# Kernel tuning notes

Measured on AMD Instinct MI355X. Metric: run time of the kernel, lower is better.

## Reference

```python
import jax, jax.numpy as jnp
import numpy as np

# Static sizes (RED-GNN on ICEWS14-like graph)
B = 32          # batch (queries)
N = 100000      # active nodes per layer (fixed frontier size)
E = 1000000     # edges per layer
H = 64          # hidden_dim
A = 5           # attn_dim
L = 3           # n_layer
N_REL = 230
N_ENT = 7128
N_TIME = 365


def setup_inputs() -> dict:
    key = jax.random.key(0)
    ks = jax.random.split(key, 16)
    inp = {}
    # edge structure (constant w.r.t. differentiation)
    inp['batch_idx'] = jax.random.randint(ks[0], (E,), 0, B)
    inp['src_idx'] = jax.random.randint(ks[1], (E,), 0, N)
    inp['dst_idx'] = jax.random.randint(ks[2], (E,), 0, N)
    inp['rel_idx'] = jax.random.randint(ks[3], (E,), 0, N_REL + 1)
    # signed relative time in [-(N_TIME-1), N_TIME-1]
    inp['rel_time'] = jax.random.randint(ks[4], (E,), -(N_TIME - 1), N_TIME)
    inp['query_rel'] = jax.random.randint(ks[5], (B,), 0, N_REL + 1)
    # unique (batch, entity) slot per final node
    n = jnp.arange(N)
    inp['out_batch'] = n // N_ENT
    inp['out_ent'] = n % N_ENT
    # learned parameters
    s = 1.0 / np.sqrt(H)
    inp['rela_embed'] = jax.random.normal(ks[6], (L, N_REL + 1, H), jnp.float32) * s
    inp['time_embed'] = jax.random.normal(ks[7], (N_TIME, H), jnp.float32) * s
    inp['Wp'] = jax.random.normal(ks[8], (H, H), jnp.float32) * s
    inp['Wn'] = jax.random.normal(ks[9], (H, H), jnp.float32) * s
    inp['Wf'] = jax.random.normal(ks[10], (H, H), jnp.float32) * s
    inp['W1'] = jax.random.normal(ks[11], (L, A, 3 * H), jnp.float32) * s
    inp['W2'] = jax.random.normal(ks[12], (L, 1, A), jnp.float32) / np.sqrt(A)
    inp['Wc'] = jax.random.normal(ks[13], (1, H), jnp.float32) * s
    inp['bc'] = jnp.zeros((1,), jnp.float32)
    return inp


def reference(rela_embed, time_embed, Wp, Wn, Wf, W1, W2, Wc, bc,
              batch_idx, src_idx, dst_idx, rel_idx, rel_time,
              query_rel, out_batch, out_ent):
    hidden = jnp.zeros((N, H), dtype=rela_embed.dtype)
    q_rel_e = query_rel[batch_idx]                 # [E]
    t_emb = time_embed[jnp.abs(rel_time)]          # [E,H]
    pos = (rel_time > 0)[:, None]
    zer = (rel_time == 0)[:, None]
    for i in range(L):
        rel_e = rela_embed[i][rel_idx]             # [E,H]
        embed = hidden[src_idx] + rel_e + t_emb    # [E,H]
        # branch by sign of relative time: future / now / past linear
        transformed = jnp.where(pos, embed @ Wf.T,
                      jnp.where(zer, embed @ Wn.T, embed @ Wp.T))
        attn_in = jnp.concatenate(
            [hidden[src_idx], rel_e, rela_embed[i][q_rel_e]], axis=1)  # [E,3H]
        score = jax.nn.sigmoid(
            jax.nn.relu(attn_in @ W1[i].T) @ W2[i].T)  # [E,1]
        msg = score * transformed                      # [E,H]
        hidden = jax.nn.relu(
            jax.ops.segment_sum(msg, dst_idx, num_segments=N))
    result = (hidden @ Wc.T + bc).reshape(-1)          # [N]
    score_all = jnp.zeros((B, N_ENT), result.dtype)
    score_all = score_all.at[out_batch, out_ent].set(result)
    return score_all
```

## Files before the change

### kernel.cpp

```cpp
#include <hip/hip_runtime.h>

#define NB   32
#define NN   100000
#define NE   1000000
#define HD   64
#define AD   5
#define NL   3
#define NRL  231
#define NTM  365
#define NOUT 228096
#define NBLK1 391
#define BLKN 32
#define NBLK2 3125


__device__ __forceinline__ float bflo(unsigned u) { return __uint_as_float(u << 16); }
__device__ __forceinline__ float bfhi(unsigned u) { return __uint_as_float(u & 0xffff0000u); }
__device__ __forceinline__ unsigned packbf2(float x, float y) {
    unsigned ux = __float_as_uint(x), uy = __float_as_uint(y);
    ux = (ux + 0x7fffu + ((ux >> 16) & 1u)) >> 16;
    uy = (uy + 0x7fffu + ((uy >> 16) & 1u)) >> 16;
    return ux | (uy << 16);
}

using vbf8  = __attribute__((ext_vector_type(8))) short;
using f32x4 = __attribute__((ext_vector_type(4))) float;

__global__ __launch_bounds__(256) void prep_wtb_kernel(
    const float* __restrict__ Wp, const float* __restrict__ Wn,
    const float* __restrict__ Wf, ushort* __restrict__ WTB)
{
    int i = blockIdx.x * 256 + threadIdx.x;
    if (i >= 3072) return;
    int lane = i & 63;
    int nt = (i >> 6) & 3;
    int ks = (i >> 8) & 1;
    int hl = (i >> 9) & 1;
    int c  = i >> 10;
    const float* W = (c == 0) ? Wf : (c == 1 ? Wn : Wp);
    int h  = nt * 16 + (lane & 15);
    int k0 = ks * 32 + (lane >> 4) * 8;
    unsigned up[4];
    #pragma unroll
    for (int j = 0; j < 4; ++j) {
        float x = W[h * 64 + k0 + 2 * j];
        float y = W[h * 64 + k0 + 2 * j + 1];
        unsigned pb = packbf2(x, y);
        if (hl) {
            float rx = x - bflo(pb);
            float ry = y - bfhi(pb);
            pb = packbf2(rx, ry);
        }
        up[j] = pb;
    }
    *(uint4*)(WTB + (size_t)i * 8) = make_uint4(up[0], up[1], up[2], up[3]);
}

__global__ __launch_bounds__(256) void prep_tb_kernel(
    const float* __restrict__ rela_embed,
    const float* __restrict__ time_embed,
    ushort* __restrict__ relb,
    ushort* __restrict__ tembb)
{
    const int nrel_w = 3 * NRL * HD / 2;
    const int ntmb_w = NTM * HD / 2;
    int i = blockIdx.x * 256 + threadIdx.x;
    if (i < nrel_w) {
        ((unsigned*)relb)[i] = packbf2(rela_embed[2 * i], rela_embed[2 * i + 1]);
    } else if (i < nrel_w + ntmb_w) {
        int k = i - nrel_w;
        ((unsigned*)tembb)[k] = packbf2(time_embed[2 * k], time_embed[2 * k + 1]);
    }
}

__global__ __launch_bounds__(256) void prep_tables_kernel(
    const float* __restrict__ rela_embed,
    const float* __restrict__ W1,
    float* __restrict__ Trel,
    float* __restrict__ Tq)
{
    int l = blockIdx.x;
    int r = threadIdx.x;
    if (r >= NRL) return;
    const float4* rrow = (const float4*)(rela_embed + ((size_t)l * NRL + r) * HD);
    const float* W1l = W1 + (size_t)l * AD * 192;
    float tr[AD] = {0,0,0,0,0}, tq[AD] = {0,0,0,0,0};
    #pragma unroll
    for (int k4 = 0; k4 < 16; ++k4) {
        float4 x = rrow[k4];
        #pragma unroll
        for (int a = 0; a < AD; ++a) {
            const float* wr = W1l + a * 192 + 64 + k4 * 4;
            const float* wq = W1l + a * 192 + 128 + k4 * 4;
            tr[a] = fmaf(x.x, wr[0], tr[a]); tr[a] = fmaf(x.y, wr[1], tr[a]);
            tr[a] = fmaf(x.z, wr[2], tr[a]); tr[a] = fmaf(x.w, wr[3], tr[a]);
            tq[a] = fmaf(x.x, wq[0], tq[a]); tq[a] = fmaf(x.y, wq[1], tq[a]);
            tq[a] = fmaf(x.z, wq[2], tq[a]); tq[a] = fmaf(x.w, wq[3], tq[a]);
        }
    }
    float* tro = Trel + ((size_t)l * NRL + r) * 8;
    float* tqo = Tq   + ((size_t)l * NRL + r) * 8;
    #pragma unroll
    for (int a = 0; a < AD; ++a) { tro[a] = tr[a]; tqo[a] = tq[a]; }
    tro[5] = tro[6] = tro[7] = 0.f;
    tqo[5] = tqo[6] = tqo[7] = 0.f;
}

__global__ __launch_bounds__(256) void hist_kernel(
    const int* __restrict__ dst_idx, int* __restrict__ deg,
    ushort* __restrict__ rank)
{
    int e = blockIdx.x * 256 + threadIdx.x;
    if (e < NE) rank[e] = (ushort)atomicAdd(&deg[dst_idx[e]], 1);
}

__global__ __launch_bounds__(256) void scan1_kernel(
    const int* __restrict__ deg, int* __restrict__ tmp, int* __restrict__ bsum)
{
    __shared__ int s[256];
    int tid = threadIdx.x;
    int i = blockIdx.x * 256 + tid;
    int v = (i < NN) ? deg[i] : 0;
    s[tid] = v;
    __syncthreads();
    #pragma unroll
    for (int st = 1; st < 256; st <<= 1) {
        int t = (tid >= st) ? s[tid - st] : 0;
        __syncthreads();
        s[tid] += t;
        __syncthreads();
    }
    if (i < NN) tmp[i] = s[tid];
    if (tid == 255) bsum[blockIdx.x] = s[255];
}

__global__ __launch_bounds__(512) void scan2_kernel(
    const int* __restrict__ bsum, int* __restrict__ bpref)
{
    __shared__ int s[512];
    int tid = threadIdx.x;
    int v = (tid < NBLK1) ? bsum[tid] : 0;
    s[tid] = v;
    __syncthreads();
    #pragma unroll
    for (int st = 1; st < 512; st <<= 1) {
        int t = (tid >= st) ? s[tid - st] : 0;
        __syncthreads();
        s[tid] += t;
        __syncthreads();
    }
    if (tid < NBLK1) bpref[tid] = s[tid] - v;
}

__global__ __launch_bounds__(256) void scan3_kernel(
    const int* __restrict__ deg, const int* __restrict__ tmp,
    const int* __restrict__ bpref, int* __restrict__ off)
{
    int i = blockIdx.x * 256 + threadIdx.x;
    if (i >= NN) return;
    int incl = tmp[i] + bpref[i >> 8];
    off[i + 1] = incl;
    if (i == 0) off[0] = 0;
}

__global__ __launch_bounds__(256) void sort_scatter_kernel(
    const int* __restrict__ dst_idx, const int* __restrict__ src_idx,
    const int* __restrict__ rel_idx, const int* __restrict__ rel_time,
    const int* __restrict__ batch_idx, const int* __restrict__ query_rel,
    const int* __restrict__ off, const ushort* __restrict__ rank,
    const float* __restrict__ Trel0, const float* __restrict__ Tq0,
    const float* __restrict__ W2,
    int2* __restrict__ meta, float* __restrict__ score0)
{
    int e = blockIdx.x * 256 + threadIdx.x;
    if (e >= NE) return;
    int d = dst_idx[e];
    int rt = rel_time[e];
    int cls = (rt > 0) ? 0 : ((rt == 0) ? 1 : 2);
    int ta = (rt < 0) ? -rt : rt;
    int rel = rel_idx[e];
    int q = query_rel[batch_idx[e]];
    int pos = off[d] + (int)rank[e];
    int2 m;
    m.x = src_idx[e] | (rel << 17) | (cls << 25);
    m.y = ta | (q << 9);
    meta[pos] = m;

    float4 t0 = *(const float4*)(Trel0 + rel * 8);
    float  t4 = Trel0[rel * 8 + 4];
    float4 u0 = *(const float4*)(Tq0 + q * 8);
    float  u4 = Tq0[q * 8 + 4];
    float z = 0.f;
    z = fmaf(fmaxf(t0.x + u0.x, 0.f), W2[0], z);
    z = fmaf(fmaxf(t0.y + u0.y, 0.f), W2[1], z);
    z = fmaf(fmaxf(t0.z + u0.z, 0.f), W2[2], z);
    z = fmaf(fmaxf(t0.w + u0.w, 0.f), W2[3], z);
    z = fmaf(fmaxf(t4   + u4,   0.f), W2[4], z);
    score0[pos] = 1.f / (1.f + __expf(-z));
}

__global__ __launch_bounds__(256) void score_kernel(
    const float* __restrict__ proj,
    const float* __restrict__ Trel,
    const float* __restrict__ Tq,
    const float* __restrict__ W2,
    const int2* __restrict__ meta,
    float* __restrict__ score)
{
    int j = blockIdx.x * 256 + threadIdx.x;
    if (j >= NE) return;
    int2 mt = meta[j];
    int rel = (mt.x >> 17) & 0xFF;
    int q   = (mt.y >> 9) & 0xFF;
    int src = mt.x & 0x1FFFF;

    float4 t0 = *(const float4*)(Trel + rel * 8);
    float  t4 = Trel[rel * 8 + 4];
    float4 u0 = *(const float4*)(Tq + q * 8);
    float  u4 = Tq[q * 8 + 4];
    float4 p0 = *(const float4*)(proj + (size_t)src * 8);
    float  p4 = proj[(size_t)src * 8 + 4];
    float z = 0.f;
    z = fmaf(fmaxf(p0.x + t0.x + u0.x, 0.f), W2[0], z);
    z = fmaf(fmaxf(p0.y + t0.y + u0.y, 0.f), W2[1], z);
    z = fmaf(fmaxf(p0.z + t0.z + u0.z, 0.f), W2[2], z);
    z = fmaf(fmaxf(p0.w + t0.w + u0.w, 0.f), W2[3], z);
    z = fmaf(fmaxf(p4   + t4   + u4,   0.f), W2[4], z);
    score[j] = 1.f / (1.f + __expf(-z));
}

template <bool HZ>
__device__ __forceinline__ void edge_acc(
    int mx, float sc, uint4 rv, uint4 tv, uint4 hv, float4* __restrict__ A)
{
    int cl = (mx >> 25) & 3;
    float4 v0, v1;
    v0.x = bflo(rv.x) + bflo(tv.x); v0.y = bfhi(rv.x) + bfhi(tv.x);
    v0.z = bflo(rv.y) + bflo(tv.y); v0.w = bfhi(rv.y) + bfhi(tv.y);
    v1.x = bflo(rv.z) + bflo(tv.z); v1.y = bfhi(rv.z) + bfhi(tv.z);
    v1.z = bflo(rv.w) + bflo(tv.w); v1.w = bfhi(rv.w) + bfhi(tv.w);
    if (!HZ) {
        v0.x += bflo(hv.x); v0.y += bfhi(hv.x);
        v0.z += bflo(hv.y); v0.w += bfhi(hv.y);
        v1.x += bflo(hv.z); v1.y += bfhi(hv.z);
        v1.z += bflo(hv.w); v1.w += bfhi(hv.w);
    }
    float sA = (cl == 0) ? sc : 0.f;
    float sB = (cl == 1) ? sc : 0.f;
    float sC = (cl == 2) ? sc : 0.f;
    A[0].x = fmaf(sA, v0.x, A[0].x); A[0].y = fmaf(sA, v0.y, A[0].y);
    A[0].z = fmaf(sA, v0.z, A[0].z); A[0].w = fmaf(sA, v0.w, A[0].w);
    A[1].x = fmaf(sA, v1.x, A[1].x); A[1].y = fmaf(sA, v1.y, A[1].y);
    A[1].z = fmaf(sA, v1.z, A[1].z); A[1].w = fmaf(sA, v1.w, A[1].w);
    A[2].x = fmaf(sB, v0.x, A[2].x); A[2].y = fmaf(sB, v0.y, A[2].y);
    A[2].z = fmaf(sB, v0.z, A[2].z); A[2].w = fmaf(sB, v0.w, A[2].w);
    A[3].x = fmaf(sB, v1.x, A[3].x); A[3].y = fmaf(sB, v1.y, A[3].y);
    A[3].z = fmaf(sB, v1.z, A[3].z); A[3].w = fmaf(sB, v1.w, A[3].w);
    A[4].x = fmaf(sC, v0.x, A[4].x); A[4].y = fmaf(sC, v0.y, A[4].y);
    A[4].z = fmaf(sC, v0.z, A[4].z); A[4].w = fmaf(sC, v0.w, A[4].w);
    A[5].x = fmaf(sC, v1.x, A[5].x); A[5].y = fmaf(sC, v1.y, A[5].y);
    A[5].z = fmaf(sC, v1.z, A[5].z); A[5].w = fmaf(sC, v1.w, A[5].w);
}

__device__ __forceinline__ uint4 ldrow(const ushort* __restrict__ base, int row, int hc8)
{
    return *(const uint4*)(base + (size_t)row * HD + hc8);
}

#define SPITCH 68
template <bool HZ, bool PROJ>
__global__ __launch_bounds__(256, 4) void reduce_transform_kernel(
    const ushort* __restrict__ hidden_in,
    const ushort* __restrict__ relb,
    const ushort* __restrict__ tembb,
    const float* __restrict__ score,
    const int2* __restrict__ meta,
    const int*  __restrict__ off,
    const ushort* __restrict__ WTB,
    const float* __restrict__ W1next,
    ushort* __restrict__ hidden_out,
    float* __restrict__ proj_out)
{
    __shared__ float lds_t[BLKN * SPITCH];
    int tid  = threadIdx.x;
    int lane = tid & 63;
    int w    = __builtin_amdgcn_readfirstlane(tid >> 6);
    int gid  = tid >> 3;
    int hc   = tid & 7;
    int hc8  = hc * 8;
    int node0 = blockIdx.x * BLKN;
    int node  = node0 + gid;

    float4 a[6];
    #pragma unroll
    for (int c = 0; c < 6; ++c)
        a[c] = make_float4(0.f, 0.f, 0.f, 0.f);

    {
        int o0 = off[node];
        int o1 = off[node + 1];
        int j = o0;
        const uint4 zz = make_uint4(0, 0, 0, 0);
        for (; j + 4 <= o1; j += 4) {
            int2 m0 = meta[j],     m1 = meta[j + 1];
            int2 m2 = meta[j + 2], m3 = meta[j + 3];
            float s0 = score[j],     s1 = score[j + 1];
            float s2 = score[j + 2], s3 = score[j + 3];
            uint4 r0 = ldrow(relb, (m0.x >> 17) & 0xFF, hc8);
            uint4 r1 = ldrow(relb, (m1.x >> 17) & 0xFF, hc8);
            uint4 r2 = ldrow(relb, (m2.x >> 17) & 0xFF, hc8);
            uint4 r3 = ldrow(relb, (m3.x >> 17) & 0xFF, hc8);
            uint4 t0 = ldrow(tembb, m0.y & 511, hc8);
            uint4 t1 = ldrow(tembb, m1.y & 511, hc8);
            uint4 t2 = ldrow(tembb, m2.y & 511, hc8);
            uint4 t3 = ldrow(tembb, m3.y & 511, hc8);
            uint4 h0 = zz, h1 = zz, h2 = zz, h3 = zz;
            if (!HZ) {
                h0 = ldrow(hidden_in, m0.x & 0x1FFFF, hc8);
                h1 = ldrow(hidden_in, m1.x & 0x1FFFF, hc8);
                h2 = ldrow(hidden_in, m2.x & 0x1FFFF, hc8);
                h3 = ldrow(hidden_in, m3.x & 0x1FFFF, hc8);
            }
            edge_acc<HZ>(m0.x, s0, r0, t0, h0, a);
            edge_acc<HZ>(m1.x, s1, r1, t1, h1, a);
            edge_acc<HZ>(m2.x, s2, r2, t2, h2, a);
            edge_acc<HZ>(m3.x, s3, r3, t3, h3, a);
        }
        for (; j < o1; ++j) {
            int2 m0 = meta[j];
            float s0 = score[j];
            uint4 r0 = ldrow(relb, (m0.x >> 17) & 0xFF, hc8);
            uint4 t0 = ldrow(tembb, m0.y & 511, hc8);
            uint4 h0 = zz;
            if (!HZ) h0 = ldrow(hidden_in, m0.x & 0x1FFFF, hc8);
            edge_acc<HZ>(m0.x, s0, r0, t0, h0, a);
        }
    }

    unsigned* lds_u = (unsigned*)lds_t;
    int rl = lane & 15;
    int t  = lane >> 4;
    int rt = w & 1;
    int ct = w >> 1;
    f32x4 accd[2];
    accd[0] = (f32x4){0.f, 0.f, 0.f, 0.f};
    accd[1] = (f32x4){0.f, 0.f, 0.f, 0.f};

    #pragma unroll
    for (int c = 0; c < 3; ++c) {
        __syncthreads();
        {
            float4 v0 = a[2 * c];
            float4 v1 = a[2 * c + 1];
            unsigned p0 = packbf2(v0.x, v0.y);
            unsigned p1 = packbf2(v0.z, v0.w);
            unsigned p2 = packbf2(v1.x, v1.y);
            unsigned p3 = packbf2(v1.z, v1.w);
            unsigned q0 = packbf2(v0.x - bflo(p0), v0.y - bfhi(p0));
            unsigned q1 = packbf2(v0.z - bflo(p1), v0.w - bfhi(p1));
            unsigned q2 = packbf2(v1.x - bflo(p2), v1.y - bfhi(p2));
            unsigned q3 = packbf2(v1.z - bflo(p3), v1.w - bfhi(p3));
            *(uint4*)(lds_u + gid * SPITCH + hc * 4)      = make_uint4(p0, p1, p2, p3);
            *(uint4*)(lds_u + gid * SPITCH + 32 + hc * 4) = make_uint4(q0, q1, q2, q3);
        }
        __syncthreads();
        #pragma unroll
        for (int ks = 0; ks < 2; ++ks) {
            const unsigned* rowp = lds_u + (rt * 16 + rl) * SPITCH + ks * 16 + t * 4;
            vbf8 ah = *(const vbf8*)rowp;
            vbf8 al = *(const vbf8*)(rowp + 32);
            #pragma unroll
            for (int b = 0; b < 2; ++b) {
                int nt = ct * 2 + b;
                const ushort* bp = WTB +
                    (size_t)((((c * 2) * 2 + ks) * 4 + nt) * 64 + lane) * 8;
                vbf8 bh = *(const vbf8*)bp;
                vbf8 bl = *(const vbf8*)(bp + 4096);
                accd[b] = __builtin_amdgcn_mfma_f32_16x16x32_bf16(ah, bh, accd[b], 0, 0, 0);
                accd[b] = __builtin_amdgcn_mfma_f32_16x16x32_bf16(al, bh, accd[b], 0, 0, 0);
                accd[b] = __builtin_amdgcn_mfma_f32_16x16x32_bf16(ah, bl, accd[b], 0, 0, 0);
            }
        }
    }

    __syncthreads();
    #pragma unroll
    for (int b = 0; b < 2; ++b)
        #pragma unroll
        for (int i = 0; i < 4; ++i)
            lds_t[(rt * 16 + t * 4 + i) * SPITCH + (ct * 2 + b) * 16 + rl] = accd[b][i];
    __syncthreads();

    float acc8[8];
    {
        const float4* rp = (const float4*)(lds_t + gid * SPITCH + hc8);
        float4 x = rp[0], y = rp[1];
        acc8[0] = x.x; acc8[1] = x.y; acc8[2] = x.z; acc8[3] = x.w;
        acc8[4] = y.x; acc8[5] = y.y; acc8[6] = y.z; acc8[7] = y.w;
    }

    {
        ushort* outp = hidden_out + (size_t)node * 64 + hc8;
        unsigned u0 = packbf2(fmaxf(acc8[0], 0.f), fmaxf(acc8[1], 0.f));
        unsigned u1 = packbf2(fmaxf(acc8[2], 0.f), fmaxf(acc8[3], 0.f));
        unsigned u2 = packbf2(fmaxf(acc8[4], 0.f), fmaxf(acc8[5], 0.f));
        unsigned u3 = packbf2(fmaxf(acc8[6], 0.f), fmaxf(acc8[7], 0.f));
        *(uint4*)outp = make_uint4(u0, u1, u2, u3);
    }

    if (PROJ) {
        float pa[AD];
        #pragma unroll
        for (int aa = 0; aa < AD; ++aa) pa[aa] = 0.f;
        #pragma unroll
        for (int i = 0; i < 8; ++i) {
            float hv = fmaxf(acc8[i], 0.f);
            #pragma unroll
            for (int aa = 0; aa < AD; ++aa)
                pa[aa] = fmaf(hv, W1next[aa * 192 + hc8 + i], pa[aa]);
        }
        __syncthreads();
        float* lds2 = lds_t;
        #pragma unroll
        for (int aa = 0; aa < AD; ++aa)
            lds2[tid * AD + aa] = pa[aa];
        __syncthreads();
        int nd = tid >> 3, aa = tid & 7;
        float v = 0.f;
        if (aa < AD) {
            #pragma unroll
            for (int ho = 0; ho < 8; ++ho)
                v += lds2[(nd * 8 + ho) * AD + aa];
        }
        proj_out[(size_t)(node0 + nd) * 8 + aa] = v;
    }
}

__global__ __launch_bounds__(256) void out_kernel(
    const ushort* __restrict__ hidden,
    const float* __restrict__ Wc,
    const float* __restrict__ bc,
    float* __restrict__ out)
{
    int i = blockIdx.x * 256 + threadIdx.x;
    if (i >= NOUT) return;
    float r = 0.f;
    if (i < NN) {
        const uint4* h4 = (const uint4*)(hidden + (size_t)i * 64);
        float acc = 0.f;
        #pragma unroll
        for (int q = 0; q < 8; ++q) {
            uint4 hv = h4[q];
            const float* wq = Wc + q * 8;
            acc = fmaf(bflo(hv.x), wq[0], acc);
            acc = fmaf(bfhi(hv.x), wq[1], acc);
            acc = fmaf(bflo(hv.y), wq[2], acc);
            acc = fmaf(bfhi(hv.y), wq[3], acc);
            acc = fmaf(bflo(hv.z), wq[4], acc);
            acc = fmaf(bfhi(hv.z), wq[5], acc);
            acc = fmaf(bflo(hv.w), wq[6], acc);
            acc = fmaf(bfhi(hv.w), wq[7], acc);
        }
        r = acc + bc[0];
    }
    out[i] = r;
}

extern "C" void kernel_launch(void* const* d_in, const int* in_sizes, int n_in,
                              void* d_out, int out_size, void* d_ws, size_t ws_size,
                              hipStream_t stream)
{
    const int*   batch_idx  = (const int*)d_in[0];
    const int*   src_idx    = (const int*)d_in[1];
    const int*   dst_idx    = (const int*)d_in[2];
    const int*   rel_idx    = (const int*)d_in[3];
    const int*   rel_time   = (const int*)d_in[4];
    const int*   query_rel  = (const int*)d_in[5];
    const float* rela_embed = (const float*)d_in[8];
    const float* time_embed = (const float*)d_in[9];
    const float* Wp         = (const float*)d_in[10];
    const float* Wn         = (const float*)d_in[11];
    const float* Wf         = (const float*)d_in[12];
    const float* W1         = (const float*)d_in[13];
    const float* W2         = (const float*)d_in[14];
    const float* Wc         = (const float*)d_in[15];
    const float* bc         = (const float*)d_in[16];
    float* out = (float*)d_out;

    char* ws = (char*)d_ws;
    ushort* hid0  = (ushort*)(ws + 0);
    ushort* hid1  = (ushort*)(ws + 12800000);
    float* projA  = (float*)(ws + 25600000);
    float* projB  = (float*)(ws + 28800000);
    float* score  = (float*)(ws + 32000000);
    ushort* WTB   = (ushort*)(ws + 36000000);
    float* Trel   = (float*)(ws + 36100000);
    float* Tq     = (float*)(ws + 36130000);
    int*   off    = (int*)  (ws + 36160000);
    int2*  meta   = (int2*) (ws + 37400000);
    int*   deg    = (int*)  (ws + 45400000);
    ushort* relb  = (ushort*)(ws + 45800000);
    ushort* tembb = (ushort*)(ws + 45950000);
    int*   tmp    = (int*)  (ws + 46600000);
    ushort* rank  = (ushort*)(ws + 47000000);
    int*   bsum   = (int*)  (ws + 49000000);
    int*   bpref  = (int*)  (ws + 49010000);

    prep_wtb_kernel<<<12, 256, 0, stream>>>(Wp, Wn, Wf, WTB);
    prep_tb_kernel<<<133, 256, 0, stream>>>(rela_embed, time_embed, relb, tembb);
    prep_tables_kernel<<<NL, 256, 0, stream>>>(rela_embed, W1, Trel, Tq);

    hipMemsetAsync(deg, 0, NN * sizeof(int), stream);
    hist_kernel<<<(NE + 255) / 256, 256, 0, stream>>>(dst_idx, deg, rank);
    scan1_kernel<<<NBLK1, 256, 0, stream>>>(deg, tmp, bsum);
    scan2_kernel<<<1, 512, 0, stream>>>(bsum, bpref);
    scan3_kernel<<<NBLK1, 256, 0, stream>>>(deg, tmp, bpref, off);
    sort_scatter_kernel<<<(NE + 255) / 256, 256, 0, stream>>>(
        dst_idx, src_idx, rel_idx, rel_time, batch_idx, query_rel,
        off, rank, Trel, Tq, W2, meta, score);

    int grid = NBLK2;
    int sgrid = (NE + 255) / 256;
    {
        reduce_transform_kernel<true, true><<<grid, 256, 0, stream>>>(
            hid1, relb, tembb, score, meta, off,
            WTB, W1 + (size_t)1 * AD * 192, hid0, projA);
    }
    {
        score_kernel<<<sgrid, 256, 0, stream>>>(
            projA, Trel + (size_t)1 * NRL * 8, Tq + (size_t)1 * NRL * 8,
            W2 + 1 * AD, meta, score);
        reduce_transform_kernel<false, true><<<grid, 256, 0, stream>>>(
            hid0, relb + (size_t)1 * NRL * HD, tembb, score, meta, off,
            WTB, W1 + (size_t)2 * AD * 192, hid1, projB);
    }
    {
        score_kernel<<<sgrid, 256, 0, stream>>>(
            projB, Trel + (size_t)2 * NRL * 8, Tq + (size_t)2 * NRL * 8,
            W2 + 2 * AD, meta, score);
        reduce_transform_kernel<false, false><<<grid, 256, 0, stream>>>(
            hid1, relb + (size_t)2 * NRL * HD, tembb, score, meta, off,
            WTB, nullptr, hid0, nullptr);
    }

    out_kernel<<<(NOUT + 255) / 256, 256, 0, stream>>>(hid0, Wc, bc, out);
}
```

Before: 380.0 us.

## Reorder nodes by in-degree to balance per-wavefront work in reduce kernel

Adds a counting sort of destination nodes by in-degree (capped at 63) producing a permutation, and makes the reduce/transform kernel process nodes in that order. Nodes sharing a wavefront then have similar edge counts, reducing divergence where lanes wait on the longest node. Costs three small extra kernels and makes hidden/proj writes scattered by row rather than contiguous per block.

```diff
diff --git a/kernel.cpp b/kernel.cpp
--- a/kernel.cpp
+++ b/kernel.cpp
@@ -161,6 +161,41 @@
     int incl = tmp[i] + bpref[i >> 8];
     off[i + 1] = incl;
     if (i == 0) off[0] = 0;
+}
+
+__global__ __launch_bounds__(256) void drank_kernel(
+    const int* __restrict__ deg, int* __restrict__ dcnt, int* __restrict__ rank_d)
+{
+    int n = blockIdx.x * 256 + threadIdx.x;
+    if (n < NN) {
+        int d = min(deg[n], 63);
+        rank_d[n] = atomicAdd(&dcnt[d], 1);
+    }
+}
+
+__global__ __launch_bounds__(64) void dscan_kernel(
+    const int* __restrict__ dcnt, int* __restrict__ dbase)
+{
+    int tid = threadIdx.x;
+    int c = dcnt[tid];
+    int v = c;
+    #pragma unroll
+    for (int st = 1; st < 64; st <<= 1) {
+        int t = __shfl_up(v, st, 64);
+        if (tid >= st) v += t;
+    }
+    dbase[tid] = v - c;
+}
+
+__global__ __launch_bounds__(256) void dscatter_kernel(
+    const int* __restrict__ deg, const int* __restrict__ rank_d,
+    const int* __restrict__ dbase, int* __restrict__ perm)
+{
+    int n = blockIdx.x * 256 + threadIdx.x;
+    if (n < NN) {
+        int d = min(deg[n], 63);
+        perm[dbase[d] + rank_d[n]] = n;
+    }
 }
 
 __global__ __launch_bounds__(256) void sort_scatter_kernel(
@@ -276,6 +311,7 @@
     const float* __restrict__ score,
     const int2* __restrict__ meta,
     const int*  __restrict__ off,
+    const int*  __restrict__ perm,
     const ushort* __restrict__ WTB,
     const float* __restrict__ W1next,
     ushort* __restrict__ hidden_out,
@@ -289,7 +325,7 @@
     int hc   = tid & 7;
     int hc8  = hc * 8;
     int node0 = blockIdx.x * BLKN;
-    int node  = node0 + gid;
+    int node  = perm[node0 + gid];
 
     float4 a[6];
     #pragma unroll
@@ -425,14 +461,13 @@
         for (int aa = 0; aa < AD; ++aa)
             lds2[tid * AD + aa] = pa[aa];
         __syncthreads();
-        int nd = tid >> 3, aa = tid & 7;
         float v = 0.f;
-        if (aa < AD) {
+        if (hc < AD) {
             #pragma unroll
             for (int ho = 0; ho < 8; ++ho)
-                v += lds2[(nd * 8 + ho) * AD + aa];
-        }
-        proj_out[(size_t)(node0 + nd) * 8 + aa] = v;
+                v += lds2[(gid * 8 + ho) * AD + hc];
+        }
+        proj_out[(size_t)node * 8 + hc] = v;
     }
 }
 
@@ -501,20 +536,27 @@
     int*   deg    = (int*)  (ws + 45400000);
     ushort* relb  = (ushort*)(ws + 45800000);
     ushort* tembb = (ushort*)(ws + 45950000);
+    int*   perm   = (int*)  (ws + 46000000);
     int*   tmp    = (int*)  (ws + 46600000);
     ushort* rank  = (ushort*)(ws + 47000000);
     int*   bsum   = (int*)  (ws + 49000000);
     int*   bpref  = (int*)  (ws + 49010000);
+    int*   dcnt   = (int*)  (ws + 49020000);
+    int*   dbase  = (int*)  (ws + 49021000);
 
     prep_wtb_kernel<<<12, 256, 0, stream>>>(Wp, Wn, Wf, WTB);
     prep_tb_kernel<<<133, 256, 0, stream>>>(rela_embed, time_embed, relb, tembb);
     prep_tables_kernel<<<NL, 256, 0, stream>>>(rela_embed, W1, Trel, Tq);
 
     hipMemsetAsync(deg, 0, NN * sizeof(int), stream);
+    hipMemsetAsync(dcnt, 0, 64 * sizeof(int), stream);
     hist_kernel<<<(NE + 255) / 256, 256, 0, stream>>>(dst_idx, deg, rank);
     scan1_kernel<<<NBLK1, 256, 0, stream>>>(deg, tmp, bsum);
     scan2_kernel<<<1, 512, 0, stream>>>(bsum, bpref);
     scan3_kernel<<<NBLK1, 256, 0, stream>>>(deg, tmp, bpref, off);
+    drank_kernel<<<NBLK1, 256, 0, stream>>>(deg, dcnt, tmp);
+    dscan_kernel<<<1, 64, 0, stream>>>(dcnt, dbase);
+    dscatter_kernel<<<NBLK1, 256, 0, stream>>>(deg, tmp, dbase, perm);
     sort_scatter_kernel<<<(NE + 255) / 256, 256, 0, stream>>>(
         dst_idx, src_idx, rel_idx, rel_time, batch_idx, query_rel,
         off, rank, Trel, Tq, W2, meta, score);
@@ -523,7 +565,7 @@
     int sgrid = (NE + 255) / 256;
     {
         reduce_transform_kernel<true, true><<<grid, 256, 0, stream>>>(
-            hid1, relb, tembb, score, meta, off,
+            hid1, relb, tembb, score, meta, off, perm,
             WTB, W1 + (size_t)1 * AD * 192, hid0, projA);
     }
     {
@@ -531,7 +573,7 @@
             projA, Trel + (size_t)1 * NRL * 8, Tq + (size_t)1 * NRL * 8,
             W2 + 1 * AD, meta, score);
         reduce_transform_kernel<false, true><<<grid, 256, 0, stream>>>(
-            hid0, relb + (size_t)1 * NRL * HD, tembb, score, meta, off,
+            hid0, relb + (size_t)1 * NRL * HD, tembb, score, meta, off, perm,
             WTB, W1 + (size_t)2 * AD * 192, hid1, projB);
     }
     {
@@ -539,7 +581,7 @@
             projB, Trel + (size_t)2 * NRL * 8, Tq + (size_t)2 * NRL * 8,
             W2 + 2 * AD, meta, score);
         reduce_transform_kernel<false, false><<<grid, 256, 0, stream>>>(
-            hid1, relb + (size_t)2 * NRL * HD, tembb, score, meta, off,
+            hid1, relb + (size_t)2 * NRL * HD, tembb, score, meta, off, perm,
             WTB, nullptr, hid0, nullptr);
     }
 
```

New measurement: 678.0 us. 1.78x slower.

## Fuse attention score computation into edge reduce kernel via lane shuffles

Applied to the files above, without the earlier changes.

Removes the separate per-edge score kernels and the score buffer; each 8-lane node group now computes the 5-dim attention pre-activation per edge (one dim per lane) from the relation, query and projected-source tables, reduces it with xor shuffles and applies the sigmoid inline. This eliminates two kernel launches and the write/read of a 1M-entry score array per layer. In exchange it adds shuffles, scattered scalar gathers of proj per edge and longer dependency chains inside the memory-bound reduce loop, and lanes 5-7 read padded table entries.

```diff
diff --git a/kernel.cpp b/kernel.cpp
--- a/kernel.cpp
+++ b/kernel.cpp
@@ -168,9 +168,7 @@
     const int* __restrict__ rel_idx, const int* __restrict__ rel_time,
     const int* __restrict__ batch_idx, const int* __restrict__ query_rel,
     const int* __restrict__ off, const ushort* __restrict__ rank,
-    const float* __restrict__ Trel0, const float* __restrict__ Tq0,
-    const float* __restrict__ W2,
-    int2* __restrict__ meta, float* __restrict__ score0)
+    int2* __restrict__ meta)
 {
     int e = blockIdx.x * 256 + threadIdx.x;
     if (e >= NE) return;
@@ -185,48 +183,6 @@
     m.x = src_idx[e] | (rel << 17) | (cls << 25);
     m.y = ta | (q << 9);
     meta[pos] = m;
-
-    float4 t0 = *(const float4*)(Trel0 + rel * 8);
-    float  t4 = Trel0[rel * 8 + 4];
-    float4 u0 = *(const float4*)(Tq0 + q * 8);
-    float  u4 = Tq0[q * 8 + 4];
-    float z = 0.f;
-    z = fmaf(fmaxf(t0.x + u0.x, 0.f), W2[0], z);
-    z = fmaf(fmaxf(t0.y + u0.y, 0.f), W2[1], z);
-    z = fmaf(fmaxf(t0.z + u0.z, 0.f), W2[2], z);
-    z = fmaf(fmaxf(t0.w + u0.w, 0.f), W2[3], z);
-    z = fmaf(fmaxf(t4   + u4,   0.f), W2[4], z);
-    score0[pos] = 1.f / (1.f + __expf(-z));
-}
-
-__global__ __launch_bounds__(256) void score_kernel(
-    const float* __restrict__ proj,
-    const float* __restrict__ Trel,
-    const float* __restrict__ Tq,
-    const float* __restrict__ W2,
-    const int2* __restrict__ meta,
-    float* __restrict__ score)
-{
-    int j = blockIdx.x * 256 + threadIdx.x;
-    if (j >= NE) return;
-    int2 mt = meta[j];
-    int rel = (mt.x >> 17) & 0xFF;
-    int q   = (mt.y >> 9) & 0xFF;
-    int src = mt.x & 0x1FFFF;
-
-    float4 t0 = *(const float4*)(Trel + rel * 8);
-    float  t4 = Trel[rel * 8 + 4];
-    float4 u0 = *(const float4*)(Tq + q * 8);
-    float  u4 = Tq[q * 8 + 4];
-    float4 p0 = *(const float4*)(proj + (size_t)src * 8);
-    float  p4 = proj[(size_t)src * 8 + 4];
-    float z = 0.f;
-    z = fmaf(fmaxf(p0.x + t0.x + u0.x, 0.f), W2[0], z);
-    z = fmaf(fmaxf(p0.y + t0.y + u0.y, 0.f), W2[1], z);
-    z = fmaf(fmaxf(p0.z + t0.z + u0.z, 0.f), W2[2], z);
-    z = fmaf(fmaxf(p0.w + t0.w + u0.w, 0.f), W2[3], z);
-    z = fmaf(fmaxf(p4   + t4   + u4,   0.f), W2[4], z);
-    score[j] = 1.f / (1.f + __expf(-z));
 }
 
 template <bool HZ>
@@ -267,13 +223,24 @@
     return *(const uint4*)(base + (size_t)row * HD + hc8);
 }
 
+__device__ __forceinline__ float grp_sigmoid(float z)
+{
+    z += __shfl_xor(z, 1);
+    z += __shfl_xor(z, 2);
+    z += __shfl_xor(z, 4);
+    return 1.f / (1.f + __expf(-z));
+}
+
 #define SPITCH 68
 template <bool HZ, bool PROJ>
 __global__ __launch_bounds__(256, 4) void reduce_transform_kernel(
     const ushort* __restrict__ hidden_in,
     const ushort* __restrict__ relb,
     const ushort* __restrict__ tembb,
-    const float* __restrict__ score,
+    const float* __restrict__ proj_in,
+    const float* __restrict__ TrelS,
+    const float* __restrict__ TqS,
+    const float* __restrict__ W2S,
     const int2* __restrict__ meta,
     const int*  __restrict__ off,
     const ushort* __restrict__ WTB,
@@ -290,6 +257,7 @@
     int hc8  = hc * 8;
     int node0 = blockIdx.x * BLKN;
     int node  = node0 + gid;
+    float w2l = (hc < AD) ? W2S[hc] : 0.f;
 
     float4 a[6];
     #pragma unroll
@@ -304,12 +272,24 @@
         for (; j + 4 <= o1; j += 4) {
             int2 m0 = meta[j],     m1 = meta[j + 1];
             int2 m2 = meta[j + 2], m3 = meta[j + 3];
-            float s0 = score[j],     s1 = score[j + 1];
-            float s2 = score[j + 2], s3 = score[j + 3];
-            uint4 r0 = ldrow(relb, (m0.x >> 17) & 0xFF, hc8);
-            uint4 r1 = ldrow(relb, (m1.x >> 17) & 0xFF, hc8);
-            uint4 r2 = ldrow(relb, (m2.x >> 17) & 0xFF, hc8);
-            uint4 r3 = ldrow(relb, (m3.x >> 17) & 0xFF, hc8);
+            int rel0 = (m0.x >> 17) & 0xFF, rel1 = (m1.x >> 17) & 0xFF;
+            int rel2 = (m2.x >> 17) & 0xFF, rel3 = (m3.x >> 17) & 0xFF;
+            int q0 = (m0.y >> 9) & 0xFF, q1 = (m1.y >> 9) & 0xFF;
+            int q2 = (m2.y >> 9) & 0xFF, q3 = (m3.y >> 9) & 0xFF;
+            float e0 = TrelS[rel0 * 8 + hc] + TqS[q0 * 8 + hc];
+            float e1 = TrelS[rel1 * 8 + hc] + TqS[q1 * 8 + hc];
+            float e2 = TrelS[rel2 * 8 + hc] + TqS[q2 * 8 + hc];
+            float e3 = TrelS[rel3 * 8 + hc] + TqS[q3 * 8 + hc];
+            if (!HZ) {
+                e0 += proj_in[(size_t)(m0.x & 0x1FFFF) * 8 + hc];
+                e1 += proj_in[(size_t)(m1.x & 0x1FFFF) * 8 + hc];
+                e2 += proj_in[(size_t)(m2.x & 0x1FFFF) * 8 + hc];
+                e3 += proj_in[(size_t)(m3.x & 0x1FFFF) * 8 + hc];
+            }
+            uint4 r0 = ldrow(relb, rel0, hc8);
+            uint4 r1 = ldrow(relb, rel1, hc8);
+            uint4 r2 = ldrow(relb, rel2, hc8);
+            uint4 r3 = ldrow(relb, rel3, hc8);
             uint4 t0 = ldrow(tembb, m0.y & 511, hc8);
             uint4 t1 = ldrow(tembb, m1.y & 511, hc8);
             uint4 t2 = ldrow(tembb, m2.y & 511, hc8);
@@ -321,19 +301,27 @@
                 h2 = ldrow(hidden_in, m2.x & 0x1FFFF, hc8);
                 h3 = ldrow(hidden_in, m3.x & 0x1FFFF, hc8);
             }
-            edge_acc<HZ>(m0.x, s0, r0, t0, h0, a);
-            edge_acc<HZ>(m1.x, s1, r1, t1, h1, a);
-            edge_acc<HZ>(m2.x, s2, r2, t2, h2, a);
-            edge_acc<HZ>(m3.x, s3, r3, t3, h3, a);
+            float sc0 = grp_sigmoid(fmaxf(e0, 0.f) * w2l);
+            float sc1 = grp_sigmoid(fmaxf(e1, 0.f) * w2l);
+            float sc2 = grp_sigmoid(fmaxf(e2, 0.f) * w2l);
+            float sc3 = grp_sigmoid(fmaxf(e3, 0.f) * w2l);
+            edge_acc<HZ>(m0.x, sc0, r0, t0, h0, a);
+            edge_acc<HZ>(m1.x, sc1, r1, t1, h1, a);
+            edge_acc<HZ>(m2.x, sc2, r2, t2, h2, a);
+            edge_acc<HZ>(m3.x, sc3, r3, t3, h3, a);
         }
         for (; j < o1; ++j) {
             int2 m0 = meta[j];
-            float s0 = score[j];
-            uint4 r0 = ldrow(relb, (m0.x >> 17) & 0xFF, hc8);
+            int rel0 = (m0.x >> 17) & 0xFF;
+            int q0 = (m0.y >> 9) & 0xFF;
+            float e0 = TrelS[rel0 * 8 + hc] + TqS[q0 * 8 + hc];
+            if (!HZ) e0 += proj_in[(size_t)(m0.x & 0x1FFFF) * 8 + hc];
+            uint4 r0 = ldrow(relb, rel0, hc8);
             uint4 t0 = ldrow(tembb, m0.y & 511, hc8);
             uint4 h0 = zz;
             if (!HZ) h0 = ldrow(hidden_in, m0.x & 0x1FFFF, hc8);
-            edge_acc<HZ>(m0.x, s0, r0, t0, h0, a);
+            float sc0 = grp_sigmoid(fmaxf(e0, 0.f) * w2l);
+            edge_acc<HZ>(m0.x, sc0, r0, t0, h0, a);
         }
     }
 
@@ -492,7 +480,6 @@
     ushort* hid1  = (ushort*)(ws + 12800000);
     float* projA  = (float*)(ws + 25600000);
     float* projB  = (float*)(ws + 28800000);
-    float* score  = (float*)(ws + 32000000);
     ushort* WTB   = (ushort*)(ws + 36000000);
     float* Trel   = (float*)(ws + 36100000);
     float* Tq     = (float*)(ws + 36130000);
@@ -517,30 +504,26 @@
     scan3_kernel<<<NBLK1, 256, 0, stream>>>(deg, tmp, bpref, off);
     sort_scatter_kernel<<<(NE + 255) / 256, 256, 0, stream>>>(
         dst_idx, src_idx, rel_idx, rel_time, batch_idx, query_rel,
-        off, rank, Trel, Tq, W2, meta, score);
+        off, rank, meta);
 
     int grid = NBLK2;
-    int sgrid = (NE + 255) / 256;
     {
         reduce_transform_kernel<true, true><<<grid, 256, 0, stream>>>(
-            hid1, relb, tembb, score, meta, off,
-            WTB, W1 + (size_t)1 * AD * 192, hid0, projA);
+            hid1, relb, tembb, nullptr,
+            Trel, Tq, W2,
+            meta, off, WTB, W1 + (size_t)1 * AD * 192, hid0, projA);
     }
     {
-        score_kernel<<<sgrid, 256, 0, stream>>>(
-            projA, Trel + (size_t)1 * NRL * 8, Tq + (size_t)1 * NRL * 8,
-            W2 + 1 * AD, meta, score);
         reduce_transform_kernel<false, true><<<grid, 256, 0, stream>>>(
-            hid0, relb + (size_t)1 * NRL * HD, tembb, score, meta, off,
-            WTB, W1 + (size_t)2 * AD * 192, hid1, projB);
+            hid0, relb + (size_t)1 * NRL * HD, tembb, projA,
+            Trel + (size_t)1 * NRL * 8, Tq + (size_t)1 * NRL * 8, W2 + 1 * AD,
+            meta, off, WTB, W1 + (size_t)2 * AD * 192, hid1, projB);
     }
     {
-        score_kernel<<<sgrid, 256, 0, stream>>>(
-            projB, Trel + (size_t)2 * NRL * 8, Tq + (size_t)2 * NRL * 8,
-            W2 + 2 * AD, meta, score);
         reduce_transform_kernel<false, false><<<grid, 256, 0, stream>>>(
-            hid1, relb + (size_t)2 * NRL * HD, tembb, score, meta, off,
-            WTB, nullptr, hid0, nullptr);
+            hid1, relb + (size_t)2 * NRL * HD, tembb, projB,
+            Trel + (size_t)2 * NRL * 8, Tq + (size_t)2 * NRL * 8, W2 + 2 * AD,
+            meta, off, WTB, nullptr, hid0, nullptr);
     }
 
     out_kernel<<<(NOUT + 255) / 256, 256, 0, stream>>>(hid0, Wc, bc, out);
```

New measurement: 434.9 us. +14.5%, slower.
